# Kernel optimization log

Measured on AMD Instinct MI355X. Metric: run time of the kernel, lower is better.

The kernel has to match this reference:

```python
import jax, jax.numpy as jnp
import numpy as np


def dct_matrix(T):
    # Orthonormal DCT-II matrix: y = D @ x  (torch_dct.dct(..., norm='ortho'))
    n = jnp.arange(T, dtype=jnp.float32)
    k = jnp.arange(T, dtype=jnp.float32)[:, None]
    D = jnp.cos(jnp.pi * (n + 0.5) * k / T) * np.sqrt(2.0 / T)
    D = D.at[0].mul(1.0 / np.sqrt(2.0))
    return D.astype(jnp.float32)


def setup_inputs() -> dict:
    key = jax.random.key(0)
    k1, k2, k3 = jax.random.split(key, 3)
    B, C, T, H, W = 8, 64, 16, 64, 64
    text_dim = 768
    r = jax.random.normal(k1, (B, C, T, H, W), dtype=jnp.float32)
    E_txt = jax.random.normal(k2, (B, text_dim), dtype=jnp.float32)
    Wf = jax.random.normal(k3, (C * T, text_dim), dtype=jnp.float32) * 0.02
    bf = jnp.zeros((C * T,), dtype=jnp.float32)
    return {"r": r, "E_txt": E_txt, "Wf": Wf, "bf": bf}


def reference(r, E_txt, Wf, bf):
    B, C, T, H, W = r.shape
    D = dct_matrix(T)  # (T, T), orthonormal so IDCT = D.T
    # DCT-II along the T axis (avoids materializing permuted copies)
    r_freq = jnp.einsum('bcthw,kt->bckhw', r, D)
    # sigmoid-gated per-(B,C,T) frequency modulation
    w = jax.nn.sigmoid((E_txt @ Wf.T + bf).reshape(B, C, T, 1, 1))
    mod = r_freq * w
    # inverse DCT (DCT-III ortho) along the frequency axis back to T
    r_out = jnp.einsum('bckhw,kt->bcthw', mod, D)
    return r_out
```

## Files before the change

### kernel.cpp

```cpp
#include <hip/hip_runtime.h>
#include <math.h>


#define HW4 1024

typedef float f4 __attribute__((ext_vector_type(4)));

__global__ __launch_bounds__(256, 4) void fused_kernel(
    const float* __restrict__ r,
    const float* __restrict__ E,
    const float* __restrict__ Wf,
    const float* __restrict__ bf,
    float* __restrict__ out)
{
    __shared__ float Dl[16][16];
    __shared__ float wv[16];
    __shared__ __align__(16) float Ms[256];

    const int tid   = threadIdx.x;
    const int wave  = tid >> 6;
    const int lane  = tid & 63;
    const int bc    = blockIdx.x >> 2;
    const int chunk = (blockIdx.x & 3) * 4 + wave;
    const int b     = bc >> 6;
    const int c     = bc & 63;
    const int krow  = tid >> 4;
    const int sub   = tid & 15;

    const size_t base = (size_t)bc * (16 * 4096);
    const f4* rp = (const f4*)(r + base);
    f4*       op = (f4*)(out + base);
    const int col = chunk * 64 + lane;

    const f4* W4 = (const f4*)Wf + (size_t)(c * 16 + krow) * 192 + sub;
    const f4* E4 = (const f4*)E + b * 192 + sub;
    float p0 = 0.f, p1 = 0.f, p2 = 0.f, p3 = 0.f;
#pragma unroll
    for (int j = 0; j < 12; j += 4) {
        f4 w0 = W4[16*(j+0)], e0 = E4[16*(j+0)];
        f4 w1 = W4[16*(j+1)], e1 = E4[16*(j+1)];
        f4 w2 = W4[16*(j+2)], e2 = E4[16*(j+2)];
        f4 w3 = W4[16*(j+3)], e3 = E4[16*(j+3)];
        p0 = fmaf(w0.x,e0.x,p0); p0 = fmaf(w0.y,e0.y,p0);
        p0 = fmaf(w0.z,e0.z,p0); p0 = fmaf(w0.w,e0.w,p0);
        p1 = fmaf(w1.x,e1.x,p1); p1 = fmaf(w1.y,e1.y,p1);
        p1 = fmaf(w1.z,e1.z,p1); p1 = fmaf(w1.w,e1.w,p1);
        p2 = fmaf(w2.x,e2.x,p2); p2 = fmaf(w2.y,e2.y,p2);
        p2 = fmaf(w2.z,e2.z,p2); p2 = fmaf(w2.w,e2.w,p2);
        p3 = fmaf(w3.x,e3.x,p3); p3 = fmaf(w3.y,e3.y,p3);
        p3 = fmaf(w3.z,e3.z,p3); p3 = fmaf(w3.w,e3.w,p3);
    }

    f4 xb[8];
#pragma unroll
    for (int k = 0; k < 8; ++k)
        xb[k] = __builtin_nontemporal_load(&rp[k * HW4 + col]);

    float p = (p0 + p1) + (p2 + p3);
    p += __shfl_xor(p, 1, 64);
    p += __shfl_xor(p, 2, 64);
    p += __shfl_xor(p, 4, 64);
    p += __shfl_xor(p, 8, 64);

    Dl[krow][sub] = (krow == 0)
        ? 0.25f
        : cospif((sub + 0.5f) * (float)krow * (1.0f / 16.0f)) * 0.35355339059327373f;
    if (sub == 0) {
        float s = p + bf[c * 16 + krow];
        wv[krow] = 1.0f / (1.0f + expf(-s));
    }
    __syncthreads();

    {
        float s = 0.f;
#pragma unroll
        for (int k = 0; k < 16; ++k)
            s = fmaf(Dl[k][krow] * wv[k], Dl[k][sub], s);
        Ms[sub * 16 + krow] = s;
    }
    __syncthreads();

    f4 y[16];
#pragma unroll
    for (int t = 0; t < 16; ++t)
        y[t] = (f4){0.f, 0.f, 0.f, 0.f};

#pragma unroll
    for (int k = 0; k < 16; ++k) {
        f4 xk = xb[k & 7];
        if (k + 8 < 16)
            xb[k & 7] = __builtin_nontemporal_load(&rp[(k + 8) * HW4 + col]);
        const f4* Mk = (const f4*)(Ms + k * 16);
#pragma unroll
        for (int t4 = 0; t4 < 4; ++t4) {
            f4 m = Mk[t4];
            y[4 * t4 + 0].x = fmaf(m.x, xk.x, y[4 * t4 + 0].x);
            y[4 * t4 + 0].y = fmaf(m.x, xk.y, y[4 * t4 + 0].y);
            y[4 * t4 + 0].z = fmaf(m.x, xk.z, y[4 * t4 + 0].z);
            y[4 * t4 + 0].w = fmaf(m.x, xk.w, y[4 * t4 + 0].w);
            y[4 * t4 + 1].x = fmaf(m.y, xk.x, y[4 * t4 + 1].x);
            y[4 * t4 + 1].y = fmaf(m.y, xk.y, y[4 * t4 + 1].y);
            y[4 * t4 + 1].z = fmaf(m.y, xk.z, y[4 * t4 + 1].z);
            y[4 * t4 + 1].w = fmaf(m.y, xk.w, y[4 * t4 + 1].w);
            y[4 * t4 + 2].x = fmaf(m.z, xk.x, y[4 * t4 + 2].x);
            y[4 * t4 + 2].y = fmaf(m.z, xk.y, y[4 * t4 + 2].y);
            y[4 * t4 + 2].z = fmaf(m.z, xk.z, y[4 * t4 + 2].z);
            y[4 * t4 + 2].w = fmaf(m.z, xk.w, y[4 * t4 + 2].w);
            y[4 * t4 + 3].x = fmaf(m.w, xk.x, y[4 * t4 + 3].x);
            y[4 * t4 + 3].y = fmaf(m.w, xk.y, y[4 * t4 + 3].y);
            y[4 * t4 + 3].z = fmaf(m.w, xk.z, y[4 * t4 + 3].z);
            y[4 * t4 + 3].w = fmaf(m.w, xk.w, y[4 * t4 + 3].w);
        }
    }

#pragma unroll
    for (int t = 0; t < 16; ++t)
        __builtin_nontemporal_store(y[t], &op[t * HW4 + col]);
}

extern "C" void kernel_launch(void* const* d_in, const int* in_sizes, int n_in,
                              void* d_out, int out_size, void* d_ws, size_t ws_size,
                              hipStream_t stream) {
    const float* r  = (const float*)d_in[0];
    const float* E  = (const float*)d_in[1];
    const float* Wf = (const float*)d_in[2];
    const float* bf = (const float*)d_in[3];
    float* out = (float*)d_out;

    fused_kernel<<<2048, 256, 0, stream>>>(r, E, Wf, bf, out);
}
```

Baseline: 240.8 us.

## Split gate/matrix computation into separate kernel from streaming modulation

Splits the fused kernel in two. A small kernel computes the per-(b,c) 16x16 combined DCT-gate-IDCT matrix once and writes it to workspace. The streaming kernel then loads that matrix and applies it to r. This removes the redundant 4x recomputation of the gate GEMV and the cosine table in every block. It also restructures the inner loop to keep all 16 inputs in registers, computing one output row at a time, and drops the nontemporal load/store hints. The cost is an extra kernel launch, a workspace round trip, and higher register pressure from holding 16 f4 inputs.

```diff
diff --git a/kernel.cpp b/kernel.cpp
--- a/kernel.cpp
+++ b/kernel.cpp
@@ -6,31 +6,20 @@
 
 typedef float f4 __attribute__((ext_vector_type(4)));
 
-__global__ __launch_bounds__(256, 4) void fused_kernel(
-    const float* __restrict__ r,
+__global__ __launch_bounds__(256) void gateM_kernel(
     const float* __restrict__ E,
     const float* __restrict__ Wf,
     const float* __restrict__ bf,
-    float* __restrict__ out)
+    float* __restrict__ Mout)
 {
     __shared__ float Dl[16][16];
     __shared__ float wv[16];
-    __shared__ __align__(16) float Ms[256];
-
-    const int tid   = threadIdx.x;
-    const int wave  = tid >> 6;
-    const int lane  = tid & 63;
-    const int bc    = blockIdx.x >> 2;
-    const int chunk = (blockIdx.x & 3) * 4 + wave;
-    const int b     = bc >> 6;
-    const int c     = bc & 63;
-    const int krow  = tid >> 4;
-    const int sub   = tid & 15;
-
-    const size_t base = (size_t)bc * (16 * 4096);
-    const f4* rp = (const f4*)(r + base);
-    f4*       op = (f4*)(out + base);
-    const int col = chunk * 64 + lane;
+    const int tid  = threadIdx.x;
+    const int bc   = blockIdx.x;
+    const int b    = bc >> 6;
+    const int c    = bc & 63;
+    const int krow = tid >> 4;
+    const int sub  = tid & 15;
 
     const f4* W4 = (const f4*)Wf + (size_t)(c * 16 + krow) * 192 + sub;
     const f4* E4 = (const f4*)E + b * 192 + sub;
@@ -50,12 +39,6 @@
         p3 = fmaf(w3.x,e3.x,p3); p3 = fmaf(w3.y,e3.y,p3);
         p3 = fmaf(w3.z,e3.z,p3); p3 = fmaf(w3.w,e3.w,p3);
     }
-
-    f4 xb[8];
-#pragma unroll
-    for (int k = 0; k < 8; ++k)
-        xb[k] = __builtin_nontemporal_load(&rp[k * HW4 + col]);
-
     float p = (p0 + p1) + (p2 + p3);
     p += __shfl_xor(p, 1, 64);
     p += __shfl_xor(p, 2, 64);
@@ -71,51 +54,56 @@
     }
     __syncthreads();
 
-    {
-        float s = 0.f;
+    float s = 0.f;
 #pragma unroll
-        for (int k = 0; k < 16; ++k)
-            s = fmaf(Dl[k][krow] * wv[k], Dl[k][sub], s);
-        Ms[sub * 16 + krow] = s;
-    }
+    for (int k = 0; k < 16; ++k)
+        s = fmaf(Dl[k][krow] * wv[k], Dl[k][sub], s);
+    Mout[bc * 256 + tid] = s;
+}
+
+__global__ __launch_bounds__(256, 4) void mod_kernel(
+    const float* __restrict__ r,
+    const float* __restrict__ M,
+    float* __restrict__ out)
+{
+    __shared__ __align__(16) float Ms[256];
+    const int tid = threadIdx.x;
+    const int bc  = blockIdx.x >> 2;
+    const int col = (blockIdx.x & 3) * 256 + tid;
+
+    const size_t base = (size_t)bc * (16 * 4096);
+    const f4* rp = (const f4*)(r + base);
+    f4*       op = (f4*)(out + base);
+
+    f4 x[16];
+#pragma unroll
+    for (int k = 0; k < 16; ++k)
+        x[k] = rp[k * HW4 + col];
+
+    if (tid < 64)
+        ((f4*)Ms)[tid] = ((const f4*)(M + bc * 256))[tid];
     __syncthreads();
 
-    f4 y[16];
 #pragma unroll
-    for (int t = 0; t < 16; ++t)
-        y[t] = (f4){0.f, 0.f, 0.f, 0.f};
-
+    for (int t = 0; t < 16; ++t) {
+        const f4* Mt = (const f4*)(Ms + t * 16);
+        f4 y = (f4){0.f, 0.f, 0.f, 0.f};
 #pragma unroll
-    for (int k = 0; k < 16; ++k) {
-        f4 xk = xb[k & 7];
-        if (k + 8 < 16)
-            xb[k & 7] = __builtin_nontemporal_load(&rp[(k + 8) * HW4 + col]);
-        const f4* Mk = (const f4*)(Ms + k * 16);
-#pragma unroll
-        for (int t4 = 0; t4 < 4; ++t4) {
-            f4 m = Mk[t4];
-            y[4 * t4 + 0].x = fmaf(m.x, xk.x, y[4 * t4 + 0].x);
-            y[4 * t4 + 0].y = fmaf(m.x, xk.y, y[4 * t4 + 0].y);
-            y[4 * t4 + 0].z = fmaf(m.x, xk.z, y[4 * t4 + 0].z);
-            y[4 * t4 + 0].w = fmaf(m.x, xk.w, y[4 * t4 + 0].w);
-            y[4 * t4 + 1].x = fmaf(m.y, xk.x, y[4 * t4 + 1].x);
-            y[4 * t4 + 1].y = fmaf(m.y, xk.y, y[4 * t4 + 1].y);
-            y[4 * t4 + 1].z = fmaf(m.y, xk.z, y[4 * t4 + 1].z);
-            y[4 * t4 + 1].w = fmaf(m.y, xk.w, y[4 * t4 + 1].w);
-            y[4 * t4 + 2].x = fmaf(m.z, xk.x, y[4 * t4 + 2].x);
-            y[4 * t4 + 2].y = fmaf(m.z, xk.y, y[4 * t4 + 2].y);
-            y[4 * t4 + 2].z = fmaf(m.z, xk.z, y[4 * t4 + 2].z);
-            y[4 * t4 + 2].w = fmaf(m.z, xk.w, y[4 * t4 + 2].w);
-            y[4 * t4 + 3].x = fmaf(m.w, xk.x, y[4 * t4 + 3].x);
-            y[4 * t4 + 3].y = fmaf(m.w, xk.y, y[4 * t4 + 3].y);
-            y[4 * t4 + 3].z = fmaf(m.w, xk.z, y[4 * t4 + 3].z);
-            y[4 * t4 + 3].w = fmaf(m.w, xk.w, y[4 * t4 + 3].w);
+        for (int k4 = 0; k4 < 4; ++k4) {
+            f4 m = Mt[k4];
+            f4 x0 = x[4*k4 + 0], x1 = x[4*k4 + 1];
+            f4 x2 = x[4*k4 + 2], x3 = x[4*k4 + 3];
+            y.x = fmaf(m.x, x0.x, y.x); y.y = fmaf(m.x, x0.y, y.y);
+            y.z = fmaf(m.x, x0.z, y.z); y.w = fmaf(m.x, x0.w, y.w);
+            y.x = fmaf(m.y, x1.x, y.x); y.y = fmaf(m.y, x1.y, y.y);
+            y.z = fmaf(m.y, x1.z, y.z); y.w = fmaf(m.y, x1.w, y.w);
+            y.x = fmaf(m.z, x2.x, y.x); y.y = fmaf(m.z, x2.y, y.y);
+            y.z = fmaf(m.z, x2.z, y.z); y.w = fmaf(m.z, x2.w, y.w);
+            y.x = fmaf(m.w, x3.x, y.x); y.y = fmaf(m.w, x3.y, y.y);
+            y.z = fmaf(m.w, x3.z, y.z); y.w = fmaf(m.w, x3.w, y.w);
         }
+        op[t * HW4 + col] = y;
     }
-
-#pragma unroll
-    for (int t = 0; t < 16; ++t)
-        __builtin_nontemporal_store(y[t], &op[t * HW4 + col]);
 }
 
 extern "C" void kernel_launch(void* const* d_in, const int* in_sizes, int n_in,
@@ -126,6 +114,8 @@
     const float* Wf = (const float*)d_in[2];
     const float* bf = (const float*)d_in[3];
     float* out = (float*)d_out;
+    float* M   = (float*)d_ws;
 
-    fused_kernel<<<2048, 256, 0, stream>>>(r, E, Wf, bf, out);
+    gateM_kernel<<<512,  256, 0, stream>>>(E, Wf, bf, M);
+    mod_kernel  <<<2048, 256, 0, stream>>>(r, M, out);
 }
```

After: 245.0 us. About the same (+1.7%).
